# Kernel tuning notes

Hardware: AMD Instinct MI355X
Metric: run time of the kernel (lower is better)

## Reference

```python
import jax, jax.numpy as jnp
import numpy as np

N, E = 50000, 800000
IN_CH, OUT_CH, HEADS, EDGE_DIM = 128, 32, 4, 16
OUT_TOTAL = OUT_CH * HEADS  # 128 == IN_CH -> skip is Identity
NEG_SLOPE = 0.2
BN_EPS = 1e-5


def setup_inputs() -> dict:
    key = jax.random.key(0)
    ks = jax.random.split(key, 12)
    s = 1.0 / np.sqrt(IN_CH)
    return {
        "x": jax.random.normal(ks[0], (N, IN_CH), jnp.float32),
        "edge_index": jax.random.randint(ks[1], (2, E), 0, N, jnp.int64),
        "edge_attr": jax.random.normal(ks[2], (E, EDGE_DIM), jnp.float32),
        # GATv2Conv params (share_weights=False): lin_l, lin_r, lin_edge, att, bias
        "W_l": jax.random.uniform(ks[3], (IN_CH, OUT_TOTAL), jnp.float32, -s, s),
        "W_r": jax.random.uniform(ks[4], (IN_CH, OUT_TOTAL), jnp.float32, -s, s),
        "W_e": jax.random.uniform(ks[5], (EDGE_DIM, OUT_TOTAL), jnp.float32, -0.25, 0.25),
        "att": jax.random.uniform(ks[6], (HEADS, OUT_CH), jnp.float32, -s, s),
        "bias": jnp.zeros((OUT_TOTAL,), jnp.float32),
        "bn_gamma": jnp.ones((OUT_TOTAL,), jnp.float32),
        "bn_beta": jnp.zeros((OUT_TOTAL,), jnp.float32),
    }


def reference(x, edge_index, edge_attr, W_l, W_r, W_e, att, bias, bn_gamma, bn_beta):
    src, dst = edge_index[0], edge_index[1]
    # GATv2Conv: per-node linear projections, reshaped to [N, H, C]
    xl = (x @ W_l).reshape(N, HEADS, OUT_CH)
    xr = (x @ W_r).reshape(N, HEADS, OUT_CH)
    # edge-wise attention input: x_l[src] + x_r[dst] + lin_edge(edge_attr)
    e = xl[src] + xr[dst] + (edge_attr @ W_e).reshape(E, HEADS, OUT_CH)
    e = jax.nn.leaky_relu(e, NEG_SLOPE)
    score = jnp.einsum('ehc,hc->eh', e, att)  # [E, H]
    # segment softmax over destination nodes
    smax = jax.ops.segment_max(score, dst, num_segments=N)
    ex = jnp.exp(score - smax[dst])
    denom = jax.ops.segment_sum(ex, dst, num_segments=N)
    alpha = ex / denom[dst]  # [E, H]
    # weighted scatter-aggregation of source features
    msg = xl[src] * alpha[:, :, None]  # [E, H, C]
    out = jax.ops.segment_sum(msg, dst, num_segments=N).reshape(N, OUT_TOTAL) + bias
    # BatchNorm1d (training-mode batch stats, biased variance)
    mu = out.mean(axis=0)
    var = out.var(axis=0)
    out = (out - mu) * jax.lax.rsqrt(var + BN_EPS) * bn_gamma + bn_beta
    out = jax.nn.elu(out)
    # dropout: eval -> identity; skip: Identity (in_channels == out_total)
    return out + x
```

## Files before the change

kernel.cpp:

```cpp
#include <hip/hip_runtime.h>
#include <math.h>

#define N_NODES 50000
#define E_EDGES 800000
#define NEG_SLOPE 0.2f
#define BN_EPS 1e-5f
#define NWAVES 8192
#define LDB 132
#define NB_SCAN 196

using bf4 = __attribute__((ext_vector_type(4))) short;
using bf8 = __attribute__((ext_vector_type(8))) short;
using f32x4 = __attribute__((ext_vector_type(4))) float;
using half2v = __attribute__((ext_vector_type(2))) _Float16;

__device__ __forceinline__ unsigned short f2b(float f) {
  unsigned u = __float_as_uint(f);
  return (unsigned short)((u + 0x7FFFu + ((u >> 16) & 1u)) >> 16);
}
__device__ __forceinline__ float b2f_lo(unsigned u) {
  return __uint_as_float(u << 16);
}
__device__ __forceinline__ float b2f_hi(unsigned u) {
  return __uint_as_float(u & 0xFFFF0000u);
}

__global__ __launch_bounds__(256) void k_projm(
    const float* __restrict__ x, const float* __restrict__ Wl,
    const float* __restrict__ Wr, unsigned short* __restrict__ xlb,
    unsigned short* __restrict__ xrb, int* __restrict__ deg,
    int* __restrict__ cur) {
  const int t = threadIdx.x;
  int gid = blockIdx.x * 256 + t;
  if (gid < N_NODES) deg[gid] = 0;
  else if (gid < 2 * N_NODES) cur[gid - N_NODES] = 0;

  __shared__ __align__(16) unsigned short blds[256 * LDB];
#pragma unroll
  for (int s = 0; s < 32; ++s) {
    int i4 = s * 256 + t;
    int k = (i4 * 4) >> 8;
    int colb = (i4 * 4) & 255;
    float4 w = (colb < 128) ? *(const float4*)(Wl + k * 128 + colb)
                            : *(const float4*)(Wr + k * 128 + (colb - 128));
    blds[(colb + 0) * LDB + k] = f2b(w.x);
    blds[(colb + 1) * LDB + k] = f2b(w.y);
    blds[(colb + 2) * LDB + k] = f2b(w.z);
    blds[(colb + 3) * LDB + k] = f2b(w.w);
  }
  __syncthreads();

  const int wave = t >> 6, lane = t & 63;
  const int f = lane & 15;
  const int g = lane >> 4;
  const int r0 = blockIdx.x * 64 + wave * 16;
  const int row = r0 + f;
  const bool rok = row < N_NODES;

  f32x4 acc[16];
#pragma unroll
  for (int c = 0; c < 16; ++c) acc[c] = (f32x4){0.f, 0.f, 0.f, 0.f};

#pragma unroll
  for (int ks = 0; ks < 4; ++ks) {
    bf8 a;
    if (rok) {
      const float* ap = x + (size_t)row * 128 + ks * 32 + g * 8;
      float4 a0 = *(const float4*)(ap);
      float4 a1 = *(const float4*)(ap + 4);
      a = (bf8){(short)f2b(a0.x), (short)f2b(a0.y), (short)f2b(a0.z),
                (short)f2b(a0.w), (short)f2b(a1.x), (short)f2b(a1.y),
                (short)f2b(a1.z), (short)f2b(a1.w)};
    } else {
      a = (bf8){0, 0, 0, 0, 0, 0, 0, 0};
    }
#pragma unroll
    for (int c = 0; c < 16; ++c) {
      const bf4* bp =
          (const bf4*)(blds + (c * 16 + f) * LDB + ks * 32 + g * 8);
      bf8 b = __builtin_shufflevector(bp[0], bp[1], 0, 1, 2, 3, 4, 5, 6, 7);
      acc[c] = __builtin_amdgcn_mfma_f32_16x16x32_bf16(a, b, acc[c], 0, 0, 0);
    }
  }

#pragma unroll
  for (int c = 0; c < 16; ++c) {
    unsigned short* dst = (c < 8) ? xlb : xrb;
    int cc = (c * 16 + f) & 127;
#pragma unroll
    for (int r = 0; r < 4; ++r) {
      int rr = r0 + g * 4 + r;
      if (rr < N_NODES) dst[(size_t)rr * 128 + cc] = f2b(acc[c][r]);
    }
  }
}

__global__ __launch_bounds__(256) void k_count(const int* __restrict__ ei,
                                               const float* __restrict__ ea,
                                               int* __restrict__ deg,
                                               int4* __restrict__ eah,
                                               float* __restrict__ bn0) {
  int t = threadIdx.x;
  if (blockIdx.x == 0) bn0[t] = 0.f;
  int e = blockIdx.x * 256 + t;
  if (e >= E_EDGES) return;
  atomicAdd(&deg[ei[E_EDGES + e]], 1);
  const float4* r = (const float4*)(ea + (size_t)e * 16);
  float4 v0 = r[0], v1 = r[1], v2 = r[2], v3 = r[3];
  union {
    half2v h[8];
    int4 q[2];
  } u;
  u.h[0] = (half2v){(_Float16)v0.x, (_Float16)v0.y};
  u.h[1] = (half2v){(_Float16)v0.z, (_Float16)v0.w};
  u.h[2] = (half2v){(_Float16)v1.x, (_Float16)v1.y};
  u.h[3] = (half2v){(_Float16)v1.z, (_Float16)v1.w};
  u.h[4] = (half2v){(_Float16)v2.x, (_Float16)v2.y};
  u.h[5] = (half2v){(_Float16)v2.z, (_Float16)v2.w};
  u.h[6] = (half2v){(_Float16)v3.x, (_Float16)v3.y};
  u.h[7] = (half2v){(_Float16)v3.z, (_Float16)v3.w};
  eah[(size_t)e * 2] = u.q[0];
  eah[(size_t)e * 2 + 1] = u.q[1];
}

__global__ __launch_bounds__(256) void k_scan_blk(const int* __restrict__ deg,
                                                  int* __restrict__ offs,
                                                  int* __restrict__ bsum) {
  __shared__ int s[256];
  int t = threadIdx.x, idx = blockIdx.x * 256 + t;
  int v = (idx < N_NODES) ? deg[idx] : 0;
  s[t] = v;
  __syncthreads();
  int acc = v;
#pragma unroll
  for (int off = 1; off < 256; off <<= 1) {
    int u = (t >= off) ? s[t - off] : 0;
    __syncthreads();
    acc += u;
    s[t] = acc;
    __syncthreads();
  }
  if (idx < N_NODES) offs[idx] = acc - v;
  if (t == 255) bsum[blockIdx.x] = acc;
}

__global__ __launch_bounds__(256) void k_scan_top(int* __restrict__ bsum) {
  __shared__ int s[256];
  int t = threadIdx.x;
  int v = (t < NB_SCAN) ? bsum[t] : 0;
  s[t] = v;
  __syncthreads();
  int acc = v;
#pragma unroll
  for (int off = 1; off < 256; off <<= 1) {
    int u = (t >= off) ? s[t - off] : 0;
    __syncthreads();
    acc += u;
    s[t] = acc;
    __syncthreads();
  }
  if (t < NB_SCAN) bsum[t] = acc - v;
}

__global__ __launch_bounds__(256) void k_scan_add(int* __restrict__ offs,
                                                  const int* __restrict__ bsum) {
  int idx = blockIdx.x * 256 + threadIdx.x;
  if (idx < N_NODES) offs[idx] += bsum[blockIdx.x];
}

__global__ __launch_bounds__(256) void k_fill(const int* __restrict__ ei,
                                              const int* __restrict__ offs,
                                              int* __restrict__ cur,
                                              int2* __restrict__ se) {
  int e = blockIdx.x * 256 + threadIdx.x;
  if (e >= E_EDGES) return;
  int d = ei[E_EDGES + e];
  int p = offs[d] + atomicAdd(&cur[d], 1);
  se[p] = make_int2(ei[e], e);
}

__device__ __forceinline__ float fscore16(const half2v* eav,
                                          const half2v* we0h,
                                          const half2v* we1h, float xrx,
                                          float xry, float ax, float ay,
                                          float xlx, float xly) {
  float xe0 = 0.f, xe1 = 0.f;
#pragma unroll
  for (int k = 0; k < 8; ++k) {
#if __has_builtin(__builtin_amdgcn_fdot2)
    xe0 = __builtin_amdgcn_fdot2(eav[k], we0h[k], xe0, false);
    xe1 = __builtin_amdgcn_fdot2(eav[k], we1h[k], xe1, false);
#else
    xe0 += (float)eav[k][0] * (float)we0h[k][0] +
           (float)eav[k][1] * (float)we0h[k][1];
    xe1 += (float)eav[k][0] * (float)we1h[k][0] +
           (float)eav[k][1] * (float)we1h[k][1];
#endif
  }
  float v0 = xlx + xrx + xe0;
  float v1 = xly + xry + xe1;
  v0 = v0 > 0.f ? v0 : NEG_SLOPE * v0;
  v1 = v1 > 0.f ? v1 : NEG_SLOPE * v1;
  float p = v0 * ax + v1 * ay;
  p += __shfl_xor(p, 1);
  p += __shfl_xor(p, 2);
  p += __shfl_xor(p, 4);
  p += __shfl_xor(p, 8);
  return p;
}

#define UPD(p, xx, xy)              \
  {                                 \
    float mn = fmaxf(m, (p));       \
    float sc = __expf(m - mn);      \
    float pe = __expf((p)-mn);      \
    den = den * sc + pe;            \
    a0 = a0 * sc + pe * (xx);       \
    a1 = a1 * sc + pe * (xy);       \
    m = mn;                         \
  }

__global__ __launch_bounds__(256, 8) void k_node(
    const unsigned short* __restrict__ xlb,
    const unsigned short* __restrict__ xrb, const int2* __restrict__ se,
    const int4* __restrict__ eah, const float* __restrict__ We,
    const float* __restrict__ att, const int* __restrict__ offs,
    const int* __restrict__ deg, float* __restrict__ out) {
  const int wid = __builtin_amdgcn_readfirstlane(
      (int)((blockIdx.x * 256 + threadIdx.x) >> 6));
  const int lane = threadIdx.x & 63;
  const int c0 = lane * 2;

  half2v we0h[8], we1h[8];
#pragma unroll
  for (int j = 0; j < 8; ++j) {
    float2 wa = *(const float2*)(We + (2 * j) * 128 + c0);
    float2 wb = *(const float2*)(We + (2 * j + 1) * 128 + c0);
    we0h[j] = (half2v){(_Float16)wa.x, (_Float16)wb.x};
    we1h[j] = (half2v){(_Float16)wa.y, (_Float16)wb.y};
  }
  float2 aw = *(const float2*)(att + c0);

  for (int d = wid; d < N_NODES; d += NWAVES) {
    const int base = __builtin_amdgcn_readfirstlane(offs[d]);
    const int n = __builtin_amdgcn_readfirstlane(deg[d]);
    unsigned ur = *(const unsigned*)(xrb + (size_t)d * 128 + c0);
    float xrx = b2f_lo(ur), xry = b2f_hi(ur);

    float m = -INFINITY, den = 0.f, a0 = 0.f, a1 = 0.f;
    int i = 0;
    for (; i + 2 <= n; i += 2) {
      int2 q0 = se[base + i];
      int2 q1 = se[base + i + 1];
      int s0 = __builtin_amdgcn_readfirstlane(q0.x);
      int s1 = __builtin_amdgcn_readfirstlane(q1.x);
      int e0 = __builtin_amdgcn_readfirstlane(q0.y);
      int e1 = __builtin_amdgcn_readfirstlane(q1.y);
      union {
        int4 q[4];
        half2v h[16];
      } u;
      u.q[0] = eah[(size_t)e0 * 2];
      u.q[1] = eah[(size_t)e0 * 2 + 1];
      u.q[2] = eah[(size_t)e1 * 2];
      u.q[3] = eah[(size_t)e1 * 2 + 1];
      unsigned uA = *(const unsigned*)(xlb + (size_t)s0 * 128 + c0);
      unsigned uB = *(const unsigned*)(xlb + (size_t)s1 * 128 + c0);
      float xAx = b2f_lo(uA), xAy = b2f_hi(uA);
      float xBx = b2f_lo(uB), xBy = b2f_hi(uB);
      float pA = fscore16(u.h, we0h, we1h, xrx, xry, aw.x, aw.y, xAx, xAy);
      float pB =
          fscore16(u.h + 8, we0h, we1h, xrx, xry, aw.x, aw.y, xBx, xBy);
      UPD(pA, xAx, xAy);
      UPD(pB, xBx, xBy);
    }
    if (i < n) {
      int2 q = se[base + i];
      int s0 = __builtin_amdgcn_readfirstlane(q.x);
      int e0 = __builtin_amdgcn_readfirstlane(q.y);
      union {
        int4 q[2];
        half2v h[8];
      } u;
      u.q[0] = eah[(size_t)e0 * 2];
      u.q[1] = eah[(size_t)e0 * 2 + 1];
      unsigned uv = *(const unsigned*)(xlb + (size_t)s0 * 128 + c0);
      float xx = b2f_lo(uv), xy = b2f_hi(uv);
      float p = fscore16(u.h, we0h, we1h, xrx, xry, aw.x, aw.y, xx, xy);
      UPD(p, xx, xy);
    }

    float inv = (n > 0) ? 1.f / den : 0.f;
    float2 o;
    o.x = a0 * inv;
    o.y = a1 * inv;
    *(float2*)(out + (size_t)d * 128 + c0) = o;
  }
}

__global__ __launch_bounds__(256) void k_bnstat(const float* __restrict__ out,
                                                float* __restrict__ bnsum,
                                                float* __restrict__ bnsq) {
  __shared__ float ls[256][4];
  __shared__ float lq[256][4];
  int t = threadIdx.x;
  int cg = t & 31;
  int rg = t >> 5;
  float s0 = 0, s1 = 0, s2 = 0, s3 = 0, q0 = 0, q1 = 0, q2 = 0, q3 = 0;
  for (int r = blockIdx.x * 8 + rg; r < N_NODES; r += gridDim.x * 8) {
    float4 v = ((const float4*)out)[(size_t)r * 32 + cg];
    s0 += v.x; s1 += v.y; s2 += v.z; s3 += v.w;
    q0 += v.x * v.x; q1 += v.y * v.y; q2 += v.z * v.z; q3 += v.w * v.w;
  }
  ls[t][0] = s0; ls[t][1] = s1; ls[t][2] = s2; ls[t][3] = s3;
  lq[t][0] = q0; lq[t][1] = q1; lq[t][2] = q2; lq[t][3] = q3;
  __syncthreads();
  if (t < 32) {
#pragma unroll
    for (int g = 1; g < 8; ++g) {
#pragma unroll
      for (int i = 0; i < 4; ++i) {
        ls[t][i] += ls[g * 32 + t][i];
        lq[t][i] += lq[g * 32 + t][i];
      }
    }
#pragma unroll
    for (int i = 0; i < 4; ++i) {
      unsafeAtomicAdd(bnsum + 4 * t + i, ls[t][i]);
      unsafeAtomicAdd(bnsq + 4 * t + i, lq[t][i]);
    }
  }
}

__global__ __launch_bounds__(256) void k_final(
    const float* __restrict__ agg, const float* __restrict__ x,
    const float* __restrict__ bnsum, const float* __restrict__ bnsq,
    const float* __restrict__ gamma, const float* __restrict__ beta,
    float* __restrict__ out) {
  __shared__ __align__(16) float ssc[128];
  __shared__ __align__(16) float ssh[128];
  int t = threadIdx.x;
  if (t < 128) {
    float mu = bnsum[t] * (1.0f / N_NODES);
    float var = bnsq[t] * (1.0f / N_NODES) - mu * mu;
    float sc = gamma[t] * rsqrtf(var + BN_EPS);
    ssc[t] = sc;
    ssh[t] = beta[t] - mu * sc;
  }
  __syncthreads();
  int i4 = blockIdx.x * 256 + t;
  if (i4 >= N_NODES * 32) return;
  int cbase = (i4 * 4) & 127;
  float4 v = ((const float4*)agg)[i4];
  float4 xv = ((const float4*)x)[i4];
  float4 sc = *(const float4*)(ssc + cbase);
  float4 sh = *(const float4*)(ssh + cbase);
  float r0 = v.x * sc.x + sh.x;
  float r1 = v.y * sc.y + sh.y;
  float r2 = v.z * sc.z + sh.z;
  float r3 = v.w * sc.w + sh.w;
  r0 = r0 > 0.f ? r0 : expm1f(r0);
  r1 = r1 > 0.f ? r1 : expm1f(r1);
  r2 = r2 > 0.f ? r2 : expm1f(r2);
  r3 = r3 > 0.f ? r3 : expm1f(r3);
  float4 o;
  o.x = r0 + xv.x; o.y = r1 + xv.y; o.z = r2 + xv.z; o.w = r3 + xv.w;
  ((float4*)out)[i4] = o;
}

extern "C" void kernel_launch(void* const* d_in, const int* in_sizes, int n_in,
                              void* d_out, int out_size, void* d_ws,
                              size_t ws_size, hipStream_t stream) {
  const float* x = (const float*)d_in[0];
  const int* ei = (const int*)d_in[1];
  const float* ea = (const float*)d_in[2];
  const float* Wl = (const float*)d_in[3];
  const float* Wr = (const float*)d_in[4];
  const float* We = (const float*)d_in[5];
  const float* att = (const float*)d_in[6];
  const float* gamma = (const float*)d_in[8];
  const float* beta = (const float*)d_in[9];
  float* out = (float*)d_out;

  unsigned short* xlb = (unsigned short*)d_ws;
  unsigned short* xrb = xlb + (size_t)N_NODES * 128;
  int* deg = (int*)(xrb + (size_t)N_NODES * 128);
  int* offs = deg + N_NODES;
  int* cur = offs + N_NODES;
  int* bsum = cur + N_NODES;
  int2* se = (int2*)(bsum + 256);
  int4* eah = (int4*)(se + E_EDGES);
  float* bnsum = (float*)(eah + (size_t)E_EDGES * 2);
  float* bnsq = bnsum + 128;

  k_projm<<<(N_NODES + 63) / 64, 256, 0, stream>>>(x, Wl, Wr, xlb, xrb, deg,
                                                   cur);
  k_count<<<(E_EDGES + 255) / 256, 256, 0, stream>>>(ei, ea, deg, eah, bnsum);
  k_scan_blk<<<NB_SCAN, 256, 0, stream>>>(deg, offs, bsum);
  k_scan_top<<<1, 256, 0, stream>>>(bsum);
  k_scan_add<<<NB_SCAN, 256, 0, stream>>>(offs, bsum);
  k_fill<<<(E_EDGES + 255) / 256, 256, 0, stream>>>(ei, offs, cur, se);
  k_node<<<NWAVES / 4, 256, 0, stream>>>(xlb, xrb, se, eah, We, att, offs,
                                         deg, out);
  k_bnstat<<<256, 256, 0, stream>>>(out, bnsum, bnsq);
  k_final<<<(N_NODES * 32 + 255) / 256, 256, 0, stream>>>(out, x, bnsum, bnsq,
                                                          gamma, beta, out);
}
```

Before: 262.7 us.

## Fuse BN statistics into node kernel, drop scan-add pass, branchy online softmax

Removes the k_scan_add launch by adding the block prefix (bsum[d>>8]) wherever offsets are read, in both k_fill and k_node. Folds the BatchNorm sum and sum-of-squares accumulation into k_node, reducing per-block through shared memory before atomics, so the separate k_bnstat pass that re-reads the 25.6MB output is gone. Rewrites the online-softmax update so each edge needs only one exp, branching on whether the running max grows. Costs are an extra bsum load per use and wave-uniform branching in the softmax update.

```diff
diff --git a/kernel.cpp b/kernel.cpp
--- a/kernel.cpp
+++ b/kernel.cpp
@@ -162,20 +162,15 @@
   if (t < NB_SCAN) bsum[t] = acc - v;
 }
 
-__global__ __launch_bounds__(256) void k_scan_add(int* __restrict__ offs,
-                                                  const int* __restrict__ bsum) {
-  int idx = blockIdx.x * 256 + threadIdx.x;
-  if (idx < N_NODES) offs[idx] += bsum[blockIdx.x];
-}
-
 __global__ __launch_bounds__(256) void k_fill(const int* __restrict__ ei,
                                               const int* __restrict__ offs,
+                                              const int* __restrict__ bsum,
                                               int* __restrict__ cur,
                                               int2* __restrict__ se) {
   int e = blockIdx.x * 256 + threadIdx.x;
   if (e >= E_EDGES) return;
   int d = ei[E_EDGES + e];
-  int p = offs[d] + atomicAdd(&cur[d], 1);
+  int p = offs[d] + bsum[d >> 8] + atomicAdd(&cur[d], 1);
   se[p] = make_int2(ei[e], e);
 }
 
@@ -209,15 +204,20 @@
   return p;
 }
 
-#define UPD(p, xx, xy)              \
-  {                                 \
-    float mn = fmaxf(m, (p));       \
-    float sc = __expf(m - mn);      \
-    float pe = __expf((p)-mn);      \
-    den = den * sc + pe;            \
-    a0 = a0 * sc + pe * (xx);       \
-    a1 = a1 * sc + pe * (xy);       \
-    m = mn;                         \
+#define UPD(p, xx, xy)                          \
+  {                                             \
+    if ((p) > m) {                              \
+      float sc = __expf(m - (p));               \
+      den = den * sc + 1.f;                     \
+      a0 = a0 * sc + (xx);                      \
+      a1 = a1 * sc + (xy);                      \
+      m = (p);                                  \
+    } else {                                    \
+      float pe = __expf((p)-m);                 \
+      den += pe;                                \
+      a0 += pe * (xx);                          \
+      a1 += pe * (xy);                          \
+    }                                           \
   }
 
 __global__ __launch_bounds__(256, 8) void k_node(
@@ -225,7 +225,9 @@
     const unsigned short* __restrict__ xrb, const int2* __restrict__ se,
     const int4* __restrict__ eah, const float* __restrict__ We,
     const float* __restrict__ att, const int* __restrict__ offs,
-    const int* __restrict__ deg, float* __restrict__ out) {
+    const int* __restrict__ bsum, const int* __restrict__ deg,
+    float* __restrict__ out, float* __restrict__ bnsum,
+    float* __restrict__ bnsq) {
   const int wid = __builtin_amdgcn_readfirstlane(
       (int)((blockIdx.x * 256 + threadIdx.x) >> 6));
   const int lane = threadIdx.x & 63;
@@ -241,8 +243,11 @@
   }
   float2 aw = *(const float2*)(att + c0);
 
+  float bs0 = 0.f, bs1 = 0.f, bq0 = 0.f, bq1 = 0.f;
+
   for (int d = wid; d < N_NODES; d += NWAVES) {
-    const int base = __builtin_amdgcn_readfirstlane(offs[d]);
+    const int base =
+        __builtin_amdgcn_readfirstlane(offs[d] + bsum[d >> 8]);
     const int n = __builtin_amdgcn_readfirstlane(deg[d]);
     unsigned ur = *(const unsigned*)(xrb + (size_t)d * 128 + c0);
     float xrx = b2f_lo(ur), xry = b2f_hi(ur);
@@ -295,40 +300,29 @@
     o.x = a0 * inv;
     o.y = a1 * inv;
     *(float2*)(out + (size_t)d * 128 + c0) = o;
-  }
-}
-
-__global__ __launch_bounds__(256) void k_bnstat(const float* __restrict__ out,
-                                                float* __restrict__ bnsum,
-                                                float* __restrict__ bnsq) {
-  __shared__ float ls[256][4];
-  __shared__ float lq[256][4];
-  int t = threadIdx.x;
-  int cg = t & 31;
-  int rg = t >> 5;
-  float s0 = 0, s1 = 0, s2 = 0, s3 = 0, q0 = 0, q1 = 0, q2 = 0, q3 = 0;
-  for (int r = blockIdx.x * 8 + rg; r < N_NODES; r += gridDim.x * 8) {
-    float4 v = ((const float4*)out)[(size_t)r * 32 + cg];
-    s0 += v.x; s1 += v.y; s2 += v.z; s3 += v.w;
-    q0 += v.x * v.x; q1 += v.y * v.y; q2 += v.z * v.z; q3 += v.w * v.w;
-  }
-  ls[t][0] = s0; ls[t][1] = s1; ls[t][2] = s2; ls[t][3] = s3;
-  lq[t][0] = q0; lq[t][1] = q1; lq[t][2] = q2; lq[t][3] = q3;
+    bs0 += o.x;
+    bs1 += o.y;
+    bq0 += o.x * o.x;
+    bq1 += o.y * o.y;
+  }
+
+  __shared__ float4 red[256];
+  red[threadIdx.x] = make_float4(bs0, bs1, bq0, bq1);
   __syncthreads();
-  if (t < 32) {
-#pragma unroll
-    for (int g = 1; g < 8; ++g) {
-#pragma unroll
-      for (int i = 0; i < 4; ++i) {
-        ls[t][i] += ls[g * 32 + t][i];
-        lq[t][i] += lq[g * 32 + t][i];
-      }
-    }
-#pragma unroll
-    for (int i = 0; i < 4; ++i) {
-      unsafeAtomicAdd(bnsum + 4 * t + i, ls[t][i]);
-      unsafeAtomicAdd(bnsq + 4 * t + i, lq[t][i]);
-    }
+  if (threadIdx.x < 64) {
+    float4 r = red[threadIdx.x];
+#pragma unroll
+    for (int w = 1; w < 4; ++w) {
+      float4 v = red[w * 64 + threadIdx.x];
+      r.x += v.x;
+      r.y += v.y;
+      r.z += v.z;
+      r.w += v.w;
+    }
+    unsafeAtomicAdd(bnsum + c0, r.x);
+    unsafeAtomicAdd(bnsum + c0 + 1, r.y);
+    unsafeAtomicAdd(bnsq + c0, r.z);
+    unsafeAtomicAdd(bnsq + c0 + 1, r.w);
   }
 }
 
@@ -398,11 +392,9 @@
   k_count<<<(E_EDGES + 255) / 256, 256, 0, stream>>>(ei, ea, deg, eah, bnsum);
   k_scan_blk<<<NB_SCAN, 256, 0, stream>>>(deg, offs, bsum);
   k_scan_top<<<1, 256, 0, stream>>>(bsum);
-  k_scan_add<<<NB_SCAN, 256, 0, stream>>>(offs, bsum);
-  k_fill<<<(E_EDGES + 255) / 256, 256, 0, stream>>>(ei, offs, cur, se);
+  k_fill<<<(E_EDGES + 255) / 256, 256, 0, stream>>>(ei, offs, bsum, cur, se);
   k_node<<<NWAVES / 4, 256, 0, stream>>>(xlb, xrb, se, eah, We, att, offs,
-                                         deg, out);
-  k_bnstat<<<256, 256, 0, stream>>>(out, bnsum, bnsq);
+                                         bsum, deg, out, bnsum, bnsq);
   k_final<<<(N_NODES * 32 + 255) / 256, 256, 0, stream>>>(out, x, bnsum, bnsq,
                                                           gamma, beta, out);
 }
```

New measurement: 302.4 us. 1.15x slower.
